# Kernel optimization log

Measured on AMD Instinct MI355X. Metric: run time of the kernel, lower is better.

The kernel has to match this reference:

```python
import jax, jax.numpy as jnp
import numpy as np
import math

D_MODEL = 512
NUM_HEADS = 8
HEAD_DIM = D_MODEL // NUM_HEADS
B, L = 2, 2048
LN_EPS = 1e-5
DEN_EPS = 1e-5


def setup_inputs() -> dict:
    key = jax.random.key(0)
    ks = jax.random.split(key, 6)
    s = 1.0 / math.sqrt(D_MODEL)
    return {
        "x": jax.random.normal(ks[0], (B, L, D_MODEL), dtype=jnp.float32),
        "Wqkv": jax.random.normal(ks[1], (D_MODEL, 3 * D_MODEL), dtype=jnp.float32) * s,
        "bqkv": jnp.zeros((3 * D_MODEL,), dtype=jnp.float32),
        "Wout": jax.random.normal(ks[2], (D_MODEL, D_MODEL), dtype=jnp.float32) * s,
        "bout": jnp.zeros((D_MODEL,), dtype=jnp.float32),
        "ln_gamma": jnp.ones((D_MODEL,), dtype=jnp.float32),
        "ln_beta": jnp.zeros((D_MODEL,), dtype=jnp.float32),
        "decay_logits": jnp.full((NUM_HEADS,), 5.0, dtype=jnp.float32),
    }


def reference(x, Wqkv, bqkv, Wout, bout, ln_gamma, ln_beta, decay_logits):
    Bv, Lv, D = x.shape
    H = decay_logits.shape[0]
    E = D // H

    qkv = x @ Wqkv + bqkv                                   # [B,L,3D]
    q, k, v = jnp.split(qkv, 3, axis=-1)
    q = q.reshape(Bv, Lv, H, E)
    k = k.reshape(Bv, Lv, H, E)
    v = v.reshape(Bv, Lv, H, E)

    # ELU feature map + 1 -> positive features; scale q by 1/sqrt(E)
    q = (jax.nn.elu(q) + 1.0) / jnp.sqrt(jnp.asarray(E, x.dtype))
    k = jax.nn.elu(k) + 1.0

    lambdas = jax.nn.sigmoid(decay_logits).reshape(1, 1, H, 1)   # [1,1,H,1]
    t = jnp.arange(Lv, dtype=x.dtype).reshape(1, Lv, 1, 1)       # [1,L,1,1]
    decay_k = jnp.power(lambdas, -t)   # lambda^{-t}
    decay_q = jnp.power(lambdas, t)    # lambda^{t}

    k_dec = k * decay_k                                          # [B,L,H,E]
    kv = jnp.einsum('blhe,blhf->blhef', k_dec, v)                # [B,L,H,E,E]
    memory = jnp.cumsum(kv, axis=1)                              # prefix-sum scan over L
    k_sum = jnp.cumsum(k_dec, axis=1)                            # [B,L,H,E]

    q_dec = q * decay_q
    num = jnp.einsum('blhe,blhef->blhf', q_dec, memory)          # [B,L,H,E]
    den = jnp.einsum('blhe,blhe->blh', q_dec, k_sum)[..., None] + DEN_EPS
    out = (num / den).reshape(Bv, Lv, D)

    out = out @ Wout + bout

    # LayerNorm (eval mode; dropout is identity)
    mu = jnp.mean(out, axis=-1, keepdims=True)
    var = jnp.var(out, axis=-1, keepdims=True)
    out = (out - mu) / jnp.sqrt(var + LN_EPS) * ln_gamma + ln_beta
    return out
```

## Files before the change

### kernel.cpp

```cpp
#include <hip/hip_runtime.h>
#include <math.h>

#define B_ 2
#define L_ 2048
#define D_ 512
#define H_ 8
#define E_ 64
#define CHUNK 32
#define NCH 64
#define DEN_EPS_ 1e-5f
#define LN_EPS_ 1e-5f

typedef __bf16 bf16x8 __attribute__((ext_vector_type(8)));
typedef __bf16 bf16x4 __attribute__((ext_vector_type(4)));
typedef float  f32x4  __attribute__((ext_vector_type(4)));

__device__ __forceinline__ float sigm(float x) { return 1.f / (1.f + expf(-x)); }
__device__ __forceinline__ float elu1(float x) { return x > 0.f ? x + 1.f : expf(x); }

__device__ __forceinline__ void async_cp16(const void* g, void* l) {
    __builtin_amdgcn_global_load_lds(
        (const __attribute__((address_space(1))) void*)g,
        (__attribute__((address_space(3))) void*)l, 16, 0, 0);
}

#define SWZ4(row, q) ((((q) ^ ((row) & 3)) * 8))

__global__ __launch_bounds__(256) void k_prep_w(
    const float* __restrict__ W1, __bf16* __restrict__ D1,
    const float* __restrict__ W2, __bf16* __restrict__ D2)
{
    const int t = threadIdx.x;
    const int bx = blockIdx.x;
    const float* src; __bf16* dst; int N, xt;
    if (bx < 24) { src = W1; dst = D1; N = 1536; xt = bx; }
    else         { src = W2; dst = D2; N = 512;  xt = bx - 24; }
    const int K = 512;

    __shared__ __bf16 tile[64][68];
    const int kb = blockIdx.y * 64, nb = xt * 64;
    const int rr = t >> 4, cc4 = (t & 15) * 4;
#pragma unroll
    for (int p = 0; p < 4; p++) {
        int k = rr + p * 16;
        float4 v = *(const float4*)&src[(size_t)(kb + k) * N + nb + cc4];
        tile[k][cc4 + 0] = (__bf16)v.x;
        tile[k][cc4 + 1] = (__bf16)v.y;
        tile[k][cc4 + 2] = (__bf16)v.z;
        tile[k][cc4 + 3] = (__bf16)v.w;
    }
    __syncthreads();
#pragma unroll
    for (int p = 0; p < 4; p++) {
        int n = rr + p * 16;
        bf16x4 o;
        o[0] = tile[cc4 + 0][n];
        o[1] = tile[cc4 + 1][n];
        o[2] = tile[cc4 + 2][n];
        o[3] = tile[cc4 + 3][n];
        *(bf16x4*)&dst[(size_t)(nb + n) * K + kb + cc4] = o;
    }
}

__global__ __launch_bounds__(256) void k_mfma_qkv(
    const float* __restrict__ X, const __bf16* __restrict__ Bt,
    const float* __restrict__ bias,
    __bf16* __restrict__ Qb, __bf16* __restrict__ Kb, __bf16* __restrict__ Vb)
{
    __shared__ __bf16 lds[12288];
    const int t = threadIdx.x;
    const int w = t >> 6, lane = t & 63;
    const int wm = w >> 1, wn = w & 1;
    const int ll = lane & 15, quad = lane >> 4;
    const int m0 = blockIdx.y * 64, n0 = blockIdx.x * 128;

    f32x4 acc[2][4] = {};
    const int sr = t >> 2;
    const int c4 = t & 3;
    const int gA = (c4 ^ (sr & 3));
    const int skz = gA * 8;

    float4 pa0, pa1;
    auto fetchA = [&](int k0) {
        const float* ap = X + (size_t)(m0 + sr) * D_ + k0 + skz;
        pa0 = *(const float4*)ap;
        pa1 = *(const float4*)(ap + 4);
    };
    auto issueB = [&](int k0, int nbuf) {
        __bf16* b0 = &lds[4096 + nbuf * 4096 + (w * 16) * 32];
        __bf16* b1 = &lds[4096 + nbuf * 4096 + (64 + w * 16) * 32];
        async_cp16(&Bt[(size_t)(n0 + sr) * D_ + k0 + skz],      b0);
        async_cp16(&Bt[(size_t)(n0 + 64 + sr) * D_ + k0 + skz], b1);
    };
    auto writeA = [&](int nbuf) {
        bf16x8 o;
        o[0] = (__bf16)pa0.x; o[1] = (__bf16)pa0.y;
        o[2] = (__bf16)pa0.z; o[3] = (__bf16)pa0.w;
        o[4] = (__bf16)pa1.x; o[5] = (__bf16)pa1.y;
        o[6] = (__bf16)pa1.z; o[7] = (__bf16)pa1.w;
        *(bf16x8*)&lds[nbuf * 2048 + sr * 32 + c4 * 8] = o;
    };

    fetchA(0);
    issueB(0, 0);
    writeA(0);
    __syncthreads();

    for (int k0 = 0; k0 < D_; k0 += 32) {
        const int buf = (k0 >> 5) & 1, nbuf = buf ^ 1;
        const int nk = k0 + 32;
        if (nk < D_) { fetchA(nk); issueB(nk, nbuf); }
        const int ao = buf * 2048, bo = 4096 + buf * 4096;
#pragma unroll
        for (int im = 0; im < 2; im++) {
            int ra = wm * 32 + im * 16 + ll;
            bf16x8 a = *(const bf16x8*)&lds[ao + ra * 32 + SWZ4(ra, quad)];
#pragma unroll
            for (int in = 0; in < 4; in++) {
                int rb = wn * 64 + in * 16 + ll;
                bf16x8 b = *(const bf16x8*)&lds[bo + rb * 32 + SWZ4(rb, quad)];
                acc[im][in] = __builtin_amdgcn_mfma_f32_16x16x32_bf16(a, b, acc[im][in], 0, 0, 0);
            }
        }
        if (nk < D_) writeA(nbuf);
        __syncthreads();
    }

    const int sec = n0 >> 9;
#pragma unroll
    for (int im = 0; im < 2; im++) {
#pragma unroll
        for (int in = 0; in < 4; in++) {
            int nc = wn * 64 + in * 16 + ll;
            float bv = bias[n0 + nc];
#pragma unroll
            for (int r = 0; r < 4; r++) {
                int mr = wm * 32 + im * 16 + quad * 4 + r;
                float v = acc[im][in][r] + bv;
                if (sec == 0)      v = elu1(v) * 0.125f;
                else if (sec == 1) v = elu1(v);
                lds[mr * 132 + nc] = (__bf16)v;
            }
        }
    }
    __syncthreads();

    __bf16* base = (sec == 0 ? Qb : (sec == 1 ? Kb : Vb));
    const int hbase = (n0 & 511) >> 6;
#pragma unroll
    for (int u = 0; u < 2; u++) {
        int id = u * 256 + t;
        int row = id >> 3;
        int c0  = (id & 7) * 16;
        bf16x8 v0 = *(bf16x8*)&lds[row * 132 + c0];
        bf16x8 v1 = *(bf16x8*)&lds[row * 132 + c0 + 8];
        int h = hbase + (c0 >> 6);
        int e0 = c0 & 63;
        int m = m0 + row, bb2 = m >> 11, l = m & 2047;
        __bf16* dst = base + ((size_t)((bb2 * H_ + h) * L_ + l)) * E_ + e0;
        *(bf16x8*)dst       = v0;
        *(bf16x8*)(dst + 8) = v1;
    }
}

__global__ __launch_bounds__(256) void k_chunk_g(
    const __bf16* __restrict__ Kb, const __bf16* __restrict__ Vb,
    const float* __restrict__ dl,
    __bf16* __restrict__ Gt, float* __restrict__ gn)
{
    __shared__ __bf16 Kwt[64][40];
    __shared__ __bf16 Vt[64][40];
    const int t  = threadIdx.x;
    const int bx = blockIdx.x;
    const int n = bx & 63, h = (bx >> 6) & 7, bb = bx >> 9;
    const int bh = bb * H_ + h;
    const float lam = sigm(dl[h]);
    const float l2  = log2f(lam);

    {
        int i = t & 31, e0 = (t >> 5) * 8;
        size_t src = ((size_t)bh * L_ + n * CHUNK + i) * E_ + e0;
        float wk = exp2f(l2 * (float)(CHUNK - 1 - i));
        bf16x8 k8 = *(const bf16x8*)&Kb[src];
        bf16x8 v8 = *(const bf16x8*)&Vb[src];
#pragma unroll
        for (int q = 0; q < 8; q++) {
            Kwt[e0 + q][i] = (__bf16)((float)k8[q] * wk);
            Vt[e0 + q][i]  = v8[q];
        }
    }
    __syncthreads();

    const int w = t >> 6, lane = t & 63;
    const int wm = w >> 1, wn = w & 1;
    const int ll = lane & 15, quad = lane >> 4;

    bf16x8 af[2], bf_[2];
#pragma unroll
    for (int a = 0; a < 2; a++) {
        af[a]  = *(const bf16x8*)&Vt[wm * 32 + a * 16 + ll][quad * 8];
        bf_[a] = *(const bf16x8*)&Kwt[wn * 32 + a * 16 + ll][quad * 8];
    }
    f32x4 acc[2][2] = {};
#pragma unroll
    for (int a = 0; a < 2; a++)
#pragma unroll
        for (int b = 0; b < 2; b++)
            acc[a][b] = __builtin_amdgcn_mfma_f32_16x16x32_bf16(af[a], bf_[b], acc[a][b], 0, 0, 0);

    size_t gbase = ((size_t)bh * NCH + n) * 4096;
#pragma unroll
    for (int a = 0; a < 2; a++)
#pragma unroll
        for (int b = 0; b < 2; b++)
#pragma unroll
            for (int r = 0; r < 4; r++) {
                int f = wm * 32 + a * 16 + quad * 4 + r;
                int e = wn * 32 + b * 16 + ll;
                Gt[gbase + (size_t)f * 64 + e] = (__bf16)acc[a][b][r];
            }

    if (t < 64) {
        float ga = 0.f;
#pragma unroll
        for (int k8 = 0; k8 < 4; k8++) {
            bf16x8 kk = *(const bf16x8*)&Kwt[t][k8 * 8];
#pragma unroll
            for (int q = 0; q < 8; q++) ga += (float)kk[q];
        }
        gn[((size_t)bh * NCH + n) * E_ + t] = ga;
    }
}

__global__ __launch_bounds__(64) void k_scan_par(
    const __bf16* __restrict__ Gt, const float* __restrict__ gn,
    const float* __restrict__ dl,
    __bf16* __restrict__ Sb, float* __restrict__ zl)
{
    const int lane = threadIdx.x;
    const int bh = blockIdx.x >> 6;
    const int j  = blockIdx.x & 63;
    const float lam = sigm(dl[bh & 7]);
    const float dC  = exp2f(32.f * log2f(lam));

    const size_t base = ((size_t)bh * NCH) * 4096 + (size_t)j * 64 + lane;

    __bf16 g[NCH];
#pragma unroll
    for (int n = 0; n < NCH; n++) g[n] = Gt[base + (size_t)n * 4096];

    float s = 0.f;
#pragma unroll
    for (int n = 0; n < NCH; n++) {
        Sb[base + (size_t)n * 4096] = (__bf16)(lam * s);
        s = fmaf(dC, s, (float)g[n]);
    }

    float gv = gn[((size_t)bh * NCH + lane) * E_ + j];
    float wf = dC;
#pragma unroll
    for (int k = 1; k < 64; k <<= 1) {
        float up = __shfl_up(gv, k);
        if (lane >= k) gv = fmaf(wf, up, gv);
        wf = wf * wf;
    }
    float zex = __shfl_up(gv, 1);
    if (lane == 0) zex = 0.f;
    zl[((size_t)bh * NCH + lane) * E_ + j] = lam * zex;
}

__global__ __launch_bounds__(256) void k_attn(
    const __bf16* __restrict__ Qb, const __bf16* __restrict__ Kb,
    const __bf16* __restrict__ Vb,
    const __bf16* __restrict__ Sb, const float* __restrict__ zl,
    const float* __restrict__ dl, __bf16* __restrict__ Out)
{
    __shared__ __bf16 Qw[32][64];
    __shared__ __bf16 Kw[32][64];
    __shared__ __bf16 Vt[64][40];
    __shared__ __bf16 A1[32][40];
    __shared__ float  den[32];
    __shared__ float  zz[64];

    const int t  = threadIdx.x;
    const int bx = blockIdx.x;
    const int n = bx & 63, h = (bx >> 6) & 7, bb = bx >> 9;
    const int bh = bb * H_ + h;
    const float lam = sigm(dl[h]);
    const float l2  = log2f(lam);

    const int w = t >> 6, lane = t & 63;
    const int ll = lane & 15, quad = lane >> 4;
    const int fw = w * 16;
    const size_t sbase = ((size_t)bh * NCH + n) * 4096;

    bf16x8 bS0 = *(const bf16x8*)&Sb[sbase + (size_t)(fw + ll) * 64 + quad * 8];
    bf16x8 bS1 = *(const bf16x8*)&Sb[sbase + (size_t)(fw + ll) * 64 + 32 + quad * 8];

    {
        int i = t >> 3, e0c = t & 7;
        size_t src = ((size_t)bh * L_ + n * CHUNK + i) * E_ + e0c * 8;
        float wq = exp2f(l2 * (float)i);
        float wk = exp2f(-l2 * (float)i);
        bf16x8 q8 = *(const bf16x8*)&Qb[src];
        bf16x8 k8 = *(const bf16x8*)&Kb[src];
        bf16x8 v8 = *(const bf16x8*)&Vb[src];
        bf16x8 qo, ko;
        int e0 = e0c * 8;
#pragma unroll
        for (int q = 0; q < 8; q++) {
            qo[q] = (__bf16)((float)q8[q] * wq);
            ko[q] = (__bf16)((float)k8[q] * wk);
            Vt[e0 + q][i] = v8[q];
        }
        int cs = (e0c ^ (i & 7)) * 8;
        *(bf16x8*)&Qw[i][cs] = qo;
        *(bf16x8*)&Kw[i][cs] = ko;
        if (t < 64) zz[t] = zl[((size_t)bh * NCH + n) * E_ + t];
    }
    __syncthreads();

    {
        const int wm = w >> 1, wn = w & 1;
        int ra = wm * 16 + ll, rb = wn * 16 + ll;
        f32x4 accA = {};
#pragma unroll
        for (int ks = 0; ks < 2; ks++) {
            bf16x8 a = *(const bf16x8*)&Qw[ra][((ks * 4 + quad) ^ (ra & 7)) * 8];
            bf16x8 b = *(const bf16x8*)&Kw[rb][((ks * 4 + quad) ^ (rb & 7)) * 8];
            accA = __builtin_amdgcn_mfma_f32_16x16x32_bf16(a, b, accA, 0, 0, 0);
        }
        int j = wn * 16 + ll;
#pragma unroll
        for (int r = 0; r < 4; r++) {
            int i = wm * 16 + quad * 4 + r;
            A1[i][j] = (__bf16)(j <= i ? accA[r] : 0.f);
        }
    }
    __syncthreads();

    if (t < 32) {
        float rs = 0.f;
#pragma unroll
        for (int k8 = 0; k8 < 4; k8++) {
            bf16x8 aa = *(const bf16x8*)&A1[t][k8 * 8];
#pragma unroll
            for (int q = 0; q < 8; q++) rs += (float)aa[q];
        }
        float qz = 0.f;
#pragma unroll
        for (int e8 = 0; e8 < 8; e8++) {
            bf16x8 qq = *(const bf16x8*)&Qw[t][(e8 ^ (t & 7)) * 8];
#pragma unroll
            for (int q = 0; q < 8; q++) qz += (float)qq[q] * zz[e8 * 8 + q];
        }
        den[t] = rs + qz + DEN_EPS_;
    }

    f32x4 acc1[2] = {}, acc2[2] = {};
    {
        bf16x8 bV = *(const bf16x8*)&Vt[fw + ll][quad * 8];
#pragma unroll
        for (int im = 0; im < 2; im++) {
            bf16x8 aA = *(const bf16x8*)&A1[im * 16 + ll][quad * 8];
            acc1[im] = __builtin_amdgcn_mfma_f32_16x16x32_bf16(aA, bV, acc1[im], 0, 0, 0);
        }
#pragma unroll
        for (int im = 0; im < 2; im++) {
            int ra = im * 16 + ll;
            bf16x8 aQ0 = *(const bf16x8*)&Qw[ra][((quad) ^ (ra & 7)) * 8];
            bf16x8 aQ1 = *(const bf16x8*)&Qw[ra][((4 + quad) ^ (ra & 7)) * 8];
            acc2[im] = __builtin_amdgcn_mfma_f32_16x16x32_bf16(aQ0, bS0, acc2[im], 0, 0, 0);
            acc2[im] = __builtin_amdgcn_mfma_f32_16x16x32_bf16(aQ1, bS1, acc2[im], 0, 0, 0);
        }
    }
    __syncthreads();

#pragma unroll
    for (int im = 0; im < 2; im++)
#pragma unroll
        for (int r = 0; r < 4; r++) {
            int i = im * 16 + quad * 4 + r;
            float o = (acc1[im][r] + acc2[im][r]) / den[i];
            Out[((size_t)bb * L_ + n * CHUNK + i) * D_ + h * E_ + fw + ll] = (__bf16)o;
        }
}

__global__ __launch_bounds__(256) void k_mfma_out_ln(
    const __bf16* __restrict__ Ab, const __bf16* __restrict__ Bt,
    const float* __restrict__ bias, const float* __restrict__ gam,
    const float* __restrict__ bet, float* __restrict__ Y)
{
    __shared__ __bf16 lds[33792];
    __shared__ float gaml[512], betl[512], bl[512];
    __shared__ float redS[4][16], redQ[4][16];
    __shared__ float mv[16][2];

    const int t = threadIdx.x;
    const int w = t >> 6, lane = t & 63;
    const int ll = lane & 15, quad = lane >> 4;
    const int m0 = blockIdx.x * 16;

    {
        float2 g = *(const float2*)&gam[t * 2];
        float2 b2 = *(const float2*)&bet[t * 2];
        float2 bo = *(const float2*)&bias[t * 2];
        gaml[t * 2] = g.x;  gaml[t * 2 + 1] = g.y;
        betl[t * 2] = b2.x; betl[t * 2 + 1] = b2.y;
        bl[t * 2]   = bo.x; bl[t * 2 + 1]   = bo.y;
    }

    f32x4 acc[8] = {};
    const int sr  = t >> 2;
    const int skz = (((t & 3) ^ (sr & 3)) * 8);

    auto issue = [&](int k0, int buf) {
        if (t < 64)
            async_cp16(&Ab[(size_t)(m0 + sr) * D_ + k0 + skz], &lds[buf * 512]);
#pragma unroll
        for (int p = 0; p < 8; p++)
            async_cp16(&Bt[(size_t)(p * 64 + sr) * D_ + k0 + skz],
                       &lds[1024 + buf * 16384 + (p * 64 + w * 16) * 32]);
    };

    issue(0, 0);
    __syncthreads();

    for (int k0 = 0; k0 < D_; k0 += 32) {
        const int buf = (k0 >> 5) & 1, nbuf = buf ^ 1;
        const int nk = k0 + 32;
        if (nk < D_) issue(nk, nbuf);
        const int ao = buf * 512, bo = 1024 + buf * 16384;
        bf16x8 a = *(const bf16x8*)&lds[ao + ll * 32 + SWZ4(ll, quad)];
#pragma unroll
        for (int in = 0; in < 8; in++) {
            int rb = w * 128 + in * 16 + ll;
            bf16x8 b = *(const bf16x8*)&lds[bo + rb * 32 + SWZ4(rb, quad)];
            acc[in] = __builtin_amdgcn_mfma_f32_16x16x32_bf16(a, b, acc[in], 0, 0, 0);
        }
        __syncthreads();
    }

    float vals[8][4];
    float ps[4] = {}, pq[4] = {};
#pragma unroll
    for (int in = 0; in < 8; in++) {
        int col = w * 128 + in * 16 + ll;
        float bv = bl[col];
#pragma unroll
        for (int r = 0; r < 4; r++) {
            float v = acc[in][r] + bv;
            vals[in][r] = v;
            ps[r] += v;
            pq[r] += v * v;
        }
    }
#pragma unroll
    for (int r = 0; r < 4; r++) {
        float s = ps[r], q = pq[r];
        s += __shfl_xor(s, 1); q += __shfl_xor(q, 1);
        s += __shfl_xor(s, 2); q += __shfl_xor(q, 2);
        s += __shfl_xor(s, 4); q += __shfl_xor(q, 4);
        s += __shfl_xor(s, 8); q += __shfl_xor(q, 8);
        if (ll == 0) {
            int row = quad * 4 + r;
            redS[w][row] = s;
            redQ[w][row] = q;
        }
    }
    __syncthreads();
    if (t < 16) {
        float S = redS[0][t] + redS[1][t] + redS[2][t] + redS[3][t];
        float Q = redQ[0][t] + redQ[1][t] + redQ[2][t] + redQ[3][t];
        float mu  = S * (1.f / 512.f);
        float var = Q * (1.f / 512.f) - mu * mu;
        mv[t][0] = mu;
        mv[t][1] = rsqrtf(var + LN_EPS_);
    }
    __syncthreads();
#pragma unroll
    for (int r = 0; r < 4; r++) {
        int row = quad * 4 + r;
        float mu = mv[row][0], rs = mv[row][1];
#pragma unroll
        for (int in = 0; in < 8; in++) {
            int col = w * 128 + in * 16 + ll;
            Y[(size_t)(m0 + row) * D_ + col] =
                (vals[in][r] - mu) * rs * gaml[col] + betl[col];
        }
    }
}

extern "C" void kernel_launch(void* const* d_in, const int* in_sizes, int n_in,
                              void* d_out, int out_size, void* d_ws, size_t ws_size,
                              hipStream_t stream)
{
    const float* x    = (const float*)d_in[0];
    const float* Wqkv = (const float*)d_in[1];
    const float* bqkv = (const float*)d_in[2];
    const float* Wout = (const float*)d_in[3];
    const float* bout = (const float*)d_in[4];
    const float* gam  = (const float*)d_in[5];
    const float* bet  = (const float*)d_in[6];
    const float* dl   = (const float*)d_in[7];
    float* out = (float*)d_out;

    const size_t NBHLE = (size_t)B_ * H_ * L_ * E_;
    const size_t NG    = (size_t)B_ * H_ * NCH * E_ * E_;
    const size_t Ng    = (size_t)B_ * H_ * NCH * E_;

    char* p = (char*)d_ws;
    __bf16* Gt  = (__bf16*)p;    p += NG * 2;
    __bf16* Sb  = (__bf16*)p;    p += NG * 2;
    float*  gn  = (float*)p;     p += Ng * 4;
    float*  zl  = (float*)p;     p += Ng * 4;
    __bf16* Qb  = (__bf16*)p;    p += NBHLE * 2;
    __bf16* Kb  = (__bf16*)p;    p += NBHLE * 2;
    __bf16* Vb  = (__bf16*)p;    p += NBHLE * 2;
    __bf16* WqkvT = (__bf16*)p;  p += (size_t)1536 * 512 * 2;
    __bf16* WoutT = (__bf16*)p;  p += (size_t)512 * 512 * 2;
    __bf16* Ao    = (__bf16*)p;  p += NBHLE * 2;

    dim3 blk(256);
    k_prep_w      <<<dim3(32, 8),  blk, 0, stream>>>(Wqkv, WqkvT, Wout, WoutT);
    k_mfma_qkv    <<<dim3(12, 64), blk, 0, stream>>>(x, WqkvT, bqkv, Qb, Kb, Vb);
    k_chunk_g     <<<dim3(1024),   blk, 0, stream>>>(Kb, Vb, dl, Gt, gn);
    k_scan_par    <<<dim3(1024),   dim3(64), 0, stream>>>(Gt, gn, dl, Sb, zl);
    k_attn        <<<dim3(1024),   blk, 0, stream>>>(Qb, Kb, Vb, Sb, zl, dl, Ao);
    k_mfma_out_ln <<<dim3(256),    blk, 0, stream>>>(Ao, WoutT, bout, gam, bet, out);
}
```

Before: 128.6 us.

## Fuse QKV projection with per-chunk K^T V state computation

The QKV GEMM kernel now computes Q, K and V columns for the same head together (three accumulator sets per block). The chunk-level K-weighted V outer-product (G) and K-sum are computed in its epilogue from LDS, which removes the separate k_chunk_g launch and its re-read of K and V from global memory. In exchange the grid shrinks from 768 to 256 blocks and LDS per block grows. The Q/K/V global stores become scalar bf16 writes instead of vectorised 16-byte stores, which may hurt coalescing and occupancy.

```diff
diff --git a/kernel.cpp b/kernel.cpp
--- a/kernel.cpp
+++ b/kernel.cpp
@@ -62,23 +62,24 @@
     }
 }
 
-__global__ __launch_bounds__(256) void k_mfma_qkv(
+__global__ __launch_bounds__(256) void k_mfma_qkv_g(
     const float* __restrict__ X, const __bf16* __restrict__ Bt,
-    const float* __restrict__ bias,
-    __bf16* __restrict__ Qb, __bf16* __restrict__ Kb, __bf16* __restrict__ Vb)
+    const float* __restrict__ bias, const float* __restrict__ dl,
+    __bf16* __restrict__ Qb, __bf16* __restrict__ Kb, __bf16* __restrict__ Vb,
+    __bf16* __restrict__ Gt, float* __restrict__ gn)
 {
-    __shared__ __bf16 lds[12288];
+    __shared__ __bf16 lds[28672];
     const int t = threadIdx.x;
     const int w = t >> 6, lane = t & 63;
     const int wm = w >> 1, wn = w & 1;
     const int ll = lane & 15, quad = lane >> 4;
     const int m0 = blockIdx.y * 64, n0 = blockIdx.x * 128;
-
-    f32x4 acc[2][4] = {};
+    const int h0 = n0 >> 6;
+
+    f32x4 acc[3][2][4] = {};
     const int sr = t >> 2;
     const int c4 = t & 3;
-    const int gA = (c4 ^ (sr & 3));
-    const int skz = gA * 8;
+    const int skz = ((c4 ^ (sr & 3)) * 8);
 
     float4 pa0, pa1;
     auto fetchA = [&](int k0) {
@@ -86,19 +87,22 @@
         pa0 = *(const float4*)ap;
         pa1 = *(const float4*)(ap + 4);
     };
-    auto issueB = [&](int k0, int nbuf) {
-        __bf16* b0 = &lds[4096 + nbuf * 4096 + (w * 16) * 32];
-        __bf16* b1 = &lds[4096 + nbuf * 4096 + (64 + w * 16) * 32];
-        async_cp16(&Bt[(size_t)(n0 + sr) * D_ + k0 + skz],      b0);
-        async_cp16(&Bt[(size_t)(n0 + 64 + sr) * D_ + k0 + skz], b1);
+    auto issueB = [&](int k0, int buf) {
+        const int bb = buf * 14336 + 2048;
+#pragma unroll
+        for (int s = 0; s < 3; s++)
+#pragma unroll
+            for (int half = 0; half < 2; half++)
+                async_cp16(&Bt[(size_t)(s * 512 + n0 + half * 64 + sr) * D_ + k0 + skz],
+                           &lds[bb + s * 4096 + (half * 64 + w * 16) * 32]);
     };
-    auto writeA = [&](int nbuf) {
+    auto writeA = [&](int buf) {
         bf16x8 o;
         o[0] = (__bf16)pa0.x; o[1] = (__bf16)pa0.y;
         o[2] = (__bf16)pa0.z; o[3] = (__bf16)pa0.w;
         o[4] = (__bf16)pa1.x; o[5] = (__bf16)pa1.y;
         o[6] = (__bf16)pa1.z; o[7] = (__bf16)pa1.w;
-        *(bf16x8*)&lds[nbuf * 2048 + sr * 32 + c4 * 8] = o;
+        *(bf16x8*)&lds[buf * 14336 + sr * 32 + c4 * 8] = o;
     };
 
     fetchA(0);
@@ -110,126 +114,113 @@
         const int buf = (k0 >> 5) & 1, nbuf = buf ^ 1;
         const int nk = k0 + 32;
         if (nk < D_) { fetchA(nk); issueB(nk, nbuf); }
-        const int ao = buf * 2048, bo = 4096 + buf * 4096;
+        const int ao = buf * 14336, bo = ao + 2048;
+        bf16x8 afr[2];
 #pragma unroll
         for (int im = 0; im < 2; im++) {
             int ra = wm * 32 + im * 16 + ll;
-            bf16x8 a = *(const bf16x8*)&lds[ao + ra * 32 + SWZ4(ra, quad)];
+            afr[im] = *(const bf16x8*)&lds[ao + ra * 32 + SWZ4(ra, quad)];
+        }
+#pragma unroll
+        for (int s = 0; s < 3; s++) {
+            bf16x8 bfr[4];
 #pragma unroll
             for (int in = 0; in < 4; in++) {
                 int rb = wn * 64 + in * 16 + ll;
-                bf16x8 b = *(const bf16x8*)&lds[bo + rb * 32 + SWZ4(rb, quad)];
-                acc[im][in] = __builtin_amdgcn_mfma_f32_16x16x32_bf16(a, b, acc[im][in], 0, 0, 0);
+                bfr[in] = *(const bf16x8*)&lds[bo + s * 4096 + rb * 32 + SWZ4(rb, quad)];
             }
+#pragma unroll
+            for (int im = 0; im < 2; im++)
+#pragma unroll
+                for (int in = 0; in < 4; in++)
+                    acc[s][im][in] = __builtin_amdgcn_mfma_f32_16x16x32_bf16(
+                        afr[im], bfr[in], acc[s][im][in], 0, 0, 0);
         }
         if (nk < D_) writeA(nbuf);
         __syncthreads();
     }
 
-    const int sec = n0 >> 9;
+    const int h = h0 + wn;
+    const float lam = sigm(dl[h]);
+    const float l2  = log2f(lam);
+    __bf16* Kwt = &lds[w * 4096];
+    __bf16* Vtw = &lds[w * 4096 + 2048];
+
+    float wk8[2][4];
+#pragma unroll
+    for (int im = 0; im < 2; im++)
+#pragma unroll
+        for (int r = 0; r < 4; r++) {
+            int i = (im * 16 + quad * 4 + r) & 31;
+            wk8[im][r] = exp2f(l2 * (float)(CHUNK - 1 - i));
+        }
+
 #pragma unroll
     for (int im = 0; im < 2; im++) {
 #pragma unroll
         for (int in = 0; in < 4; in++) {
             int nc = wn * 64 + in * 16 + ll;
-            float bv = bias[n0 + nc];
+            int e  = nc & 63;
+            float bq = bias[n0 + nc];
+            float bk = bias[512 + n0 + nc];
+            float bv = bias[1024 + n0 + nc];
 #pragma unroll
             for (int r = 0; r < 4; r++) {
                 int mr = wm * 32 + im * 16 + quad * 4 + r;
-                float v = acc[im][in][r] + bv;
-                if (sec == 0)      v = elu1(v) * 0.125f;
-                else if (sec == 1) v = elu1(v);
-                lds[mr * 132 + nc] = (__bf16)v;
+                int m = m0 + mr, bb2 = m >> 11, l = m & 2047;
+                size_t off = ((size_t)((bb2 * H_ + h) * L_ + l)) * E_ + e;
+                float vq = elu1(acc[0][im][in][r] + bq) * 0.125f;
+                float vk = elu1(acc[1][im][in][r] + bk);
+                float vv = acc[2][im][in][r] + bv;
+                Qb[off] = (__bf16)vq;
+                Kb[off] = (__bf16)vk;
+                Vb[off] = (__bf16)vv;
+                int i = mr & 31;
+                int col = ((i >> 3) ^ (e & 3)) * 8 + (i & 7);
+                Kwt[e * 32 + col] = (__bf16)(vk * wk8[im][r]);
+                Vtw[e * 32 + col] = (__bf16)vv;
             }
         }
     }
-    __syncthreads();
-
-    __bf16* base = (sec == 0 ? Qb : (sec == 1 ? Kb : Vb));
-    const int hbase = (n0 & 511) >> 6;
-#pragma unroll
-    for (int u = 0; u < 2; u++) {
-        int id = u * 256 + t;
-        int row = id >> 3;
-        int c0  = (id & 7) * 16;
-        bf16x8 v0 = *(bf16x8*)&lds[row * 132 + c0];
-        bf16x8 v1 = *(bf16x8*)&lds[row * 132 + c0 + 8];
-        int h = hbase + (c0 >> 6);
-        int e0 = c0 & 63;
-        int m = m0 + row, bb2 = m >> 11, l = m & 2047;
-        __bf16* dst = base + ((size_t)((bb2 * H_ + h) * L_ + l)) * E_ + e0;
-        *(bf16x8*)dst       = v0;
-        *(bf16x8*)(dst + 8) = v1;
-    }
-}
-
-__global__ __launch_bounds__(256) void k_chunk_g(
-    const __bf16* __restrict__ Kb, const __bf16* __restrict__ Vb,
-    const float* __restrict__ dl,
-    __bf16* __restrict__ Gt, float* __restrict__ gn)
-{
-    __shared__ __bf16 Kwt[64][40];
-    __shared__ __bf16 Vt[64][40];
-    const int t  = threadIdx.x;
-    const int bx = blockIdx.x;
-    const int n = bx & 63, h = (bx >> 6) & 7, bb = bx >> 9;
-    const int bh = bb * H_ + h;
-    const float lam = sigm(dl[h]);
-    const float l2  = log2f(lam);
+
+    const int bb2 = m0 >> 11;
+    const int bh = bb2 * H_ + h;
+    const int nchunk = ((m0 & 2047) >> 5) + wm;
 
     {
-        int i = t & 31, e0 = (t >> 5) * 8;
-        size_t src = ((size_t)bh * L_ + n * CHUNK + i) * E_ + e0;
-        float wk = exp2f(l2 * (float)(CHUNK - 1 - i));
-        bf16x8 k8 = *(const bf16x8*)&Kb[src];
-        bf16x8 v8 = *(const bf16x8*)&Vb[src];
-#pragma unroll
-        for (int q = 0; q < 8; q++) {
-            Kwt[e0 + q][i] = (__bf16)((float)k8[q] * wk);
-            Vt[e0 + q][i]  = v8[q];
-        }
-    }
-    __syncthreads();
-
-    const int w = t >> 6, lane = t & 63;
-    const int wm = w >> 1, wn = w & 1;
-    const int ll = lane & 15, quad = lane >> 4;
-
-    bf16x8 af[2], bf_[2];
-#pragma unroll
-    for (int a = 0; a < 2; a++) {
-        af[a]  = *(const bf16x8*)&Vt[wm * 32 + a * 16 + ll][quad * 8];
-        bf_[a] = *(const bf16x8*)&Kwt[wn * 32 + a * 16 + ll][quad * 8];
-    }
-    f32x4 acc[2][2] = {};
-#pragma unroll
-    for (int a = 0; a < 2; a++)
-#pragma unroll
-        for (int b = 0; b < 2; b++)
-            acc[a][b] = __builtin_amdgcn_mfma_f32_16x16x32_bf16(af[a], bf_[b], acc[a][b], 0, 0, 0);
-
-    size_t gbase = ((size_t)bh * NCH + n) * 4096;
-#pragma unroll
-    for (int a = 0; a < 2; a++)
-#pragma unroll
-        for (int b = 0; b < 2; b++)
+        float ga = 0.f;
+#pragma unroll
+        for (int ci = 0; ci < 4; ci++) {
+            int colb = ((ci ^ (lane & 3)) * 8);
+#pragma unroll
+            for (int j = 0; j < 8; j++) ga += (float)Kwt[lane * 32 + colb + j];
+        }
+        gn[((size_t)bh * NCH + nchunk) * E_ + lane] = ga;
+    }
+
+    f32x4 gac[4][4] = {};
+#pragma unroll
+    for (int a = 0; a < 4; a++) {
+        int raf = a * 16 + ll;
+        bf16x8 av = *(const bf16x8*)&Vtw[raf * 32 + SWZ4(raf, quad)];
+#pragma unroll
+        for (int b2 = 0; b2 < 4; b2++) {
+            int rbe = b2 * 16 + ll;
+            bf16x8 kv = *(const bf16x8*)&Kwt[rbe * 32 + SWZ4(rbe, quad)];
+            gac[a][b2] = __builtin_amdgcn_mfma_f32_16x16x32_bf16(av, kv, gac[a][b2], 0, 0, 0);
+        }
+    }
+    size_t gbase = ((size_t)bh * NCH + nchunk) * 4096;
+#pragma unroll
+    for (int a = 0; a < 4; a++)
+#pragma unroll
+        for (int b2 = 0; b2 < 4; b2++)
 #pragma unroll
             for (int r = 0; r < 4; r++) {
-                int f = wm * 32 + a * 16 + quad * 4 + r;
-                int e = wn * 32 + b * 16 + ll;
-                Gt[gbase + (size_t)f * 64 + e] = (__bf16)acc[a][b][r];
+                int f = a * 16 + quad * 4 + r;
+                int e = b2 * 16 + ll;
+                Gt[gbase + (size_t)f * 64 + e] = (__bf16)gac[a][b2][r];
             }
-
-    if (t < 64) {
-        float ga = 0.f;
-#pragma unroll
-        for (int k8 = 0; k8 < 4; k8++) {
-            bf16x8 kk = *(const bf16x8*)&Kwt[t][k8 * 8];
-#pragma unroll
-            for (int q = 0; q < 8; q++) ga += (float)kk[q];
-        }
-        gn[((size_t)bh * NCH + n) * E_ + t] = ga;
-    }
 }
 
 __global__ __launch_bounds__(64) void k_scan_par(
@@ -522,10 +513,10 @@
     __bf16* Ao    = (__bf16*)p;  p += NBHLE * 2;
 
     dim3 blk(256);
-    k_prep_w      <<<dim3(32, 8),  blk, 0, stream>>>(Wqkv, WqkvT, Wout, WoutT);
-    k_mfma_qkv    <<<dim3(12, 64), blk, 0, stream>>>(x, WqkvT, bqkv, Qb, Kb, Vb);
-    k_chunk_g     <<<dim3(1024),   blk, 0, stream>>>(Kb, Vb, dl, Gt, gn);
-    k_scan_par    <<<dim3(1024),   dim3(64), 0, stream>>>(Gt, gn, dl, Sb, zl);
-    k_attn        <<<dim3(1024),   blk, 0, stream>>>(Qb, Kb, Vb, Sb, zl, dl, Ao);
-    k_mfma_out_ln <<<dim3(256),    blk, 0, stream>>>(Ao, WoutT, bout, gam, bet, out);
-}
+    k_prep_w      <<<dim3(32, 8), blk, 0, stream>>>(Wqkv, WqkvT, Wout, WoutT);
+    k_mfma_qkv_g  <<<dim3(4, 64), blk, 0, stream>>>(x, WqkvT, bqkv, dl,
+                                                    Qb, Kb, Vb, Gt, gn);
+    k_scan_par    <<<dim3(1024),  dim3(64), 0, stream>>>(Gt, gn, dl, Sb, zl);
+    k_attn        <<<dim3(1024),  blk, 0, stream>>>(Qb, Kb, Vb, Sb, zl, dl, Ao);
+    k_mfma_out_ln <<<dim3(256),   blk, 0, stream>>>(Ao, WoutT, bout, gam, bet, out);
+}
```

New measurement: 128.6 us. No clear change (-0.0%).
